# Optimization experiments

Hardware: AMD Instinct MI355X
Metric: run time of the kernel (lower is better)

## Reference

```python
import jax, jax.numpy as jnp
import numpy as np

EMBED_DIM = 1024
HEAD_DIM = 64
B, S = 16, 2048


def setup_inputs() -> dict:
    key = jax.random.key(0)
    ks = jax.random.split(key, 8)
    scale = 1.0 / np.sqrt(EMBED_DIM)
    return {
        "x": jax.random.normal(ks[0], (B, S, EMBED_DIM), dtype=jnp.float32),
        "mask": jax.random.randint(ks[1], (B, S), 0, 2, dtype=jnp.int32),
        "Wq": jax.random.normal(ks[2], (EMBED_DIM, HEAD_DIM), dtype=jnp.float32) * scale,
        "bq": jnp.zeros((HEAD_DIM,), dtype=jnp.float32),
        "Wk": jax.random.normal(ks[3], (EMBED_DIM, HEAD_DIM), dtype=jnp.float32) * scale,
        "bk": jnp.zeros((HEAD_DIM,), dtype=jnp.float32),
        "Wv": jax.random.normal(ks[4], (EMBED_DIM, HEAD_DIM), dtype=jnp.float32) * scale,
        "bv": jnp.zeros((HEAD_DIM,), dtype=jnp.float32),
    }


def reference(x, mask, Wq, bq, Wk, bk, Wv, bv):
    # x: [B,S,E], mask: [B,S] with 0 = masked, 1 = keep
    q = x @ Wq + bq          # [B,S,D]
    k = x @ Wk + bk          # [B,S,D]
    v = x @ Wv + bv          # [B,S,D]
    scores = jnp.einsum("bsd,btd->bst", q, k) / jnp.sqrt(jnp.float32(HEAD_DIM))
    scores = jnp.where(mask[:, None, :] == 0, jnp.float32(-1e9), scores)
    attn = jax.nn.softmax(scores, axis=-1)  # [B,S,S]
    return jnp.einsum("bst,btd->bsd", attn, v)  # [B,S,D]
```

## Files before the change

### kernel.cpp

```cpp
#include <hip/hip_runtime.h>
#include <math.h>

#define EMBED 1024
#define HDIM  64
#define BATCH 16
#define SEQ   2048
#define MTOT  (BATCH*SEQ)
#define NE    (MTOT*HDIM)

typedef _Float16 f16;
typedef __attribute__((ext_vector_type(8))) _Float16 half8;
typedef __attribute__((ext_vector_type(4))) _Float16 half4;
typedef __attribute__((ext_vector_type(4))) float  float4v;

__global__ void wprep_kernel(const float* __restrict__ Wq, const float* __restrict__ Wk,
                             const float* __restrict__ Wv, f16* __restrict__ Wt)
{
    int e = blockIdx.x * 256 + threadIdx.x;
    if (e >= 192 * EMBED) return;
    int gn = e >> 10, k = e & 1023;
    int mat = gn >> 6, n = gn & 63;
    const float* W = (mat == 0) ? Wq : ((mat == 1) ? Wk : Wv);
    Wt[e] = (f16)W[k * HDIM + n];
}

__global__ __launch_bounds__(256)
void qkv_mfma_kernel(const float* __restrict__ X, const f16* __restrict__ Wt,
                     const float* __restrict__ bq, const float* __restrict__ bk, const float* __restrict__ bv,
                     f16* __restrict__ Q, f16* __restrict__ K, f16* __restrict__ Vt)
{
    __shared__ f16 Xs[64 * 72];
    __shared__ f16 Csv[64 * 72];

    const int tid  = threadIdx.x;
    const int wave = tid >> 6;
    const int lane = tid & 63;
    const int quad = lane >> 4;
    const int c16  = lane & 15;
    const int m0   = blockIdx.x * 64;
    const int gnb  = wave * 3;

    float4v acc[4][3];
    #pragma unroll
    for (int mt = 0; mt < 4; ++mt)
        #pragma unroll
        for (int nt = 0; nt < 3; ++nt)
            acc[mt][nt] = (float4v){0.f, 0.f, 0.f, 0.f};

    float4 pf[4];
    #pragma unroll
    for (int i = 0; i < 4; ++i) {
        int c = tid + 256 * i, m = c >> 4, ko = (c & 15) * 4;
        pf[i] = *(const float4*)(X + (size_t)(m0 + m) * EMBED + ko);
    }

    for (int k0 = 0; k0 < EMBED; k0 += 64) {
        half8 bh[2][3];
        #pragma unroll
        for (int ks = 0; ks < 2; ++ks)
            #pragma unroll
            for (int nt = 0; nt < 3; ++nt)
                bh[ks][nt] = *(const half8*)(Wt + (size_t)((gnb + nt) * 16 + c16) * EMBED
                                             + k0 + ks * 32 + quad * 8);

        __syncthreads();
        #pragma unroll
        for (int i = 0; i < 4; ++i) {
            int c = tid + 256 * i, m = c >> 4, ko = (c & 15) * 4;
            half4 h = { (f16)pf[i].x, (f16)pf[i].y, (f16)pf[i].z, (f16)pf[i].w };
            *(half4*)&Xs[m * 72 + ko] = h;
        }
        __syncthreads();

        {
            int k1 = (k0 + 64) & (EMBED - 1);
            #pragma unroll
            for (int i = 0; i < 4; ++i) {
                int c = tid + 256 * i, m = c >> 4, ko = (c & 15) * 4;
                pf[i] = *(const float4*)(X + (size_t)(m0 + m) * EMBED + k1 + ko);
            }
        }

        #pragma unroll
        for (int ks = 0; ks < 2; ++ks) {
            half8 a[4];
            #pragma unroll
            for (int mt = 0; mt < 4; ++mt)
                a[mt] = *(const half8*)&Xs[(mt * 16 + c16) * 72 + ks * 32 + quad * 8];
            #pragma unroll
            for (int mt = 0; mt < 4; ++mt)
                #pragma unroll
                for (int nt = 0; nt < 3; ++nt)
                    acc[mt][nt] = __builtin_amdgcn_mfma_f32_16x16x32_f16(a[mt], bh[ks][nt], acc[mt][nt], 0, 0, 0);
        }
    }

    float bb[3];
    #pragma unroll
    for (int nt = 0; nt < 3; ++nt) {
        int gn = (gnb + nt) * 16 + c16, mat = gn >> 6, cn = gn & 63;
        bb[nt] = ((mat == 0) ? bq : ((mat == 1) ? bk : bv))[cn];
    }

    #pragma unroll
    for (int mt = 0; mt < 4; ++mt)
        #pragma unroll
        for (int nt = 0; nt < 3; ++nt) {
            int gn = (gnb + nt) * 16 + c16, mat = gn >> 6, cn = gn & 63;
            if (mat < 2) {
                f16* O = mat ? K : Q;
                #pragma unroll
                for (int r = 0; r < 4; ++r)
                    O[(size_t)(m0 + mt * 16 + quad * 4 + r) * HDIM + cn] =
                        (f16)(acc[mt][nt][r] + bb[nt]);
            }
        }

    __syncthreads();
    #pragma unroll
    for (int mt = 0; mt < 4; ++mt)
        #pragma unroll
        for (int nt = 0; nt < 3; ++nt) {
            int gn = (gnb + nt) * 16 + c16, mat = gn >> 6, cn = gn & 63;
            if (mat == 2) {
                #pragma unroll
                for (int r = 0; r < 4; ++r)
                    Csv[cn * 72 + mt * 16 + quad * 4 + r] = (f16)(acc[mt][nt][r] + bb[nt]);
            }
        }
    __syncthreads();
    {
        int d = tid >> 2, ms = (tid & 3) * 16;
        #pragma unroll
        for (int j = 0; j < 2; ++j)
            *(half8*)(Vt + (size_t)d * MTOT + m0 + ms + 8 * j) =
                *(const half8*)&Csv[d * 72 + ms + 8 * j];
    }
}

__global__ __launch_bounds__(256)
void attn_mfma_kernel(const f16* __restrict__ Q, const f16* __restrict__ K,
                      const f16* __restrict__ Vt, const int* __restrict__ mask,
                      float* __restrict__ out)
{
    __shared__ f16 Ks[64 * 72];
    __shared__ f16 Vs[64 * 72];
    __shared__ f16 Ps[4 * 16 * 72];
    __shared__ int maskS[64];

    const int tid  = threadIdx.x;
    const int wave = tid >> 6;
    const int lane = tid & 63;
    const int quad = lane >> 4;
    const int c16  = lane & 15;
    const int b    = blockIdx.y;
    const int s0   = blockIdx.x * 64;
    const int q0   = s0 + wave * 16;

    const size_t qrow = (size_t)(b * SEQ + q0 + c16) * HDIM;
    half8 qa0 = *(const half8*)(Q + qrow + quad * 8);
    half8 qa1 = *(const half8*)(Q + qrow + 32 + quad * 8);

    const half8 ones = { (f16)1.f, (f16)1.f, (f16)1.f, (f16)1.f,
                         (f16)1.f, (f16)1.f, (f16)1.f, (f16)1.f };

    float4v O[4];
    #pragma unroll
    for (int dt = 0; dt < 4; ++dt) O[dt] = (float4v){0.f, 0.f, 0.f, 0.f};
    float4v lacc = (float4v){0.f, 0.f, 0.f, 0.f};

    const size_t kbase = (size_t)b * SEQ * HDIM;
    const int vcol0 = b * SEQ;
    const int pbase = wave * 16 * 72;

    half8 pfK[2], pfV[2];
    int mreg;
    #pragma unroll
    for (int i = 0; i < 2; ++i) {
        int c = tid + 256 * i, j = c >> 3, o = (c & 7) * 8;
        pfK[i] = *(const half8*)(K  + kbase + (size_t)j * HDIM + o);
        pfV[i] = *(const half8*)(Vt + (size_t)j * MTOT + vcol0 + o);
    }
    mreg = mask[b * SEQ + (tid & 63)];

    for (int t0 = 0; t0 < SEQ; t0 += 64) {
        __syncthreads();
        #pragma unroll
        for (int i = 0; i < 2; ++i) {
            int c = tid + 256 * i, j = c >> 3, o = (c & 7) * 8;
            *(half8*)&Ks[j * 72 + o] = pfK[i];
            *(half8*)&Vs[j * 72 + o] = pfV[i];
        }
        if (tid < 64) maskS[tid] = mreg;
        __syncthreads();

        {
            int t1 = (t0 + 64) & (SEQ - 1);
            #pragma unroll
            for (int i = 0; i < 2; ++i) {
                int c = tid + 256 * i, j = c >> 3, o = (c & 7) * 8;
                pfK[i] = *(const half8*)(K  + kbase + (size_t)(t1 + j) * HDIM + o);
                pfV[i] = *(const half8*)(Vt + (size_t)j * MTOT + vcol0 + t1 + o);
            }
            mreg = mask[b * SEQ + t1 + (tid & 63)];
        }

        float4v s[4];
        #pragma unroll
        for (int nt = 0; nt < 4; ++nt) {
            const int krow = (nt * 16 + c16) * 72;
            half8 kh0 = *(const half8*)&Ks[krow + quad * 8];
            half8 kh1 = *(const half8*)&Ks[krow + 32 + quad * 8];
            float4v a = (float4v){0.f, 0.f, 0.f, 0.f};
            a = __builtin_amdgcn_mfma_f32_16x16x32_f16(qa0, kh0, a, 0, 0, 0);
            a = __builtin_amdgcn_mfma_f32_16x16x32_f16(qa1, kh1, a, 0, 0, 0);
            s[nt] = a;
        }

        #pragma unroll
        for (int nt = 0; nt < 4; ++nt) {
            int mk = maskS[nt * 16 + c16];
            #pragma unroll
            for (int r = 0; r < 4; ++r) {
                float t = fmaf(s[nt][r], 0.125f, -6.0f);
                t = mk ? t : -1e30f;
                Ps[pbase + (quad * 4 + r) * 72 + nt * 16 + c16] = (f16)__expf(t);
            }
        }

        const int prow = pbase + c16 * 72;
        half8 pa0 = *(const half8*)&Ps[prow + quad * 8];
        half8 pa1 = *(const half8*)&Ps[prow + 32 + quad * 8];
        lacc = __builtin_amdgcn_mfma_f32_16x16x32_f16(pa0, ones, lacc, 0, 0, 0);
        lacc = __builtin_amdgcn_mfma_f32_16x16x32_f16(pa1, ones, lacc, 0, 0, 0);
        #pragma unroll
        for (int dt = 0; dt < 4; ++dt) {
            const int vrow = (dt * 16 + c16) * 72;
            half8 vh0 = *(const half8*)&Vs[vrow + quad * 8];
            half8 vh1 = *(const half8*)&Vs[vrow + 32 + quad * 8];
            O[dt] = __builtin_amdgcn_mfma_f32_16x16x32_f16(pa0, vh0, O[dt], 0, 0, 0);
            O[dt] = __builtin_amdgcn_mfma_f32_16x16x32_f16(pa1, vh1, O[dt], 0, 0, 0);
        }
    }

    #pragma unroll
    for (int r = 0; r < 4; ++r) {
        float inv = 1.0f / lacc[r];
        size_t orow = (size_t)(b * SEQ + q0 + quad * 4 + r) * HDIM;
        #pragma unroll
        for (int dt = 0; dt < 4; ++dt)
            out[orow + dt * 16 + c16] = O[dt][r] * inv;
    }
}

extern "C" void kernel_launch(void* const* d_in, const int* in_sizes, int n_in,
                              void* d_out, int out_size, void* d_ws, size_t ws_size,
                              hipStream_t stream) {
    const float* x    = (const float*)d_in[0];
    const int*   mask = (const int*)  d_in[1];
    const float* Wq   = (const float*)d_in[2];
    const float* bq   = (const float*)d_in[3];
    const float* Wk   = (const float*)d_in[4];
    const float* bk   = (const float*)d_in[5];
    const float* Wv   = (const float*)d_in[6];
    const float* bv   = (const float*)d_in[7];
    float* out = (float*)d_out;

    f16* Qf = (f16*)d_ws;
    f16* Kf = Qf + (size_t)NE;
    f16* Vt = Kf + (size_t)NE;
    f16* Wt = Vt + (size_t)NE;

    wprep_kernel<<<dim3(768), dim3(256), 0, stream>>>(Wq, Wk, Wv, Wt);

    qkv_mfma_kernel<<<dim3(MTOT / 64), dim3(256), 0, stream>>>(
        x, Wt, bq, bk, bv, Qf, Kf, Vt);

    attn_mfma_kernel<<<dim3(SEQ / 64, BATCH), dim3(256), 0, stream>>>(
        Qf, Kf, Vt, mask, out);
}
```

Before: 261.4 us.

## Give each attention wave two query tiles and double-buffer K/V in LDS

The attention kernel drops from 4 waves of 16 query rows to 2 waves of 32 rows each, so every K/V fragment read from LDS feeds two MFMA tiles. K/V shared buffers are double-buffered, which removes one of the two block barriers per key tile. The mask now lives in registers and is broadcast with wave shuffles instead of going through LDS. The cost is higher register pressure per wave, fewer waves per block (so less latency hiding), and more LDS use.

```diff
diff --git a/kernel.cpp b/kernel.cpp
--- a/kernel.cpp
+++ b/kernel.cpp
@@ -138,15 +138,14 @@
     }
 }
 
-__global__ __launch_bounds__(256)
+__global__ __launch_bounds__(128)
 void attn_mfma_kernel(const f16* __restrict__ Q, const f16* __restrict__ K,
                       const f16* __restrict__ Vt, const int* __restrict__ mask,
                       float* __restrict__ out)
 {
-    __shared__ f16 Ks[64 * 72];
-    __shared__ f16 Vs[64 * 72];
-    __shared__ f16 Ps[4 * 16 * 72];
-    __shared__ int maskS[64];
+    __shared__ f16 Ks[2][64 * 72];
+    __shared__ f16 Vs[2][64 * 72];
+    __shared__ f16 Ps[2][32 * 72];
 
     const int tid  = threadIdx.x;
     const int wave = tid >> 6;
@@ -155,102 +154,131 @@
     const int c16  = lane & 15;
     const int b    = blockIdx.y;
     const int s0   = blockIdx.x * 64;
-    const int q0   = s0 + wave * 16;
-
-    const size_t qrow = (size_t)(b * SEQ + q0 + c16) * HDIM;
-    half8 qa0 = *(const half8*)(Q + qrow + quad * 8);
-    half8 qa1 = *(const half8*)(Q + qrow + 32 + quad * 8);
+    const int q0   = s0 + wave * 32;
+
+    half8 qa[2][2];
+    #pragma unroll
+    for (int qt = 0; qt < 2; ++qt) {
+        const size_t qrow = (size_t)(b * SEQ + q0 + qt * 16 + c16) * HDIM;
+        qa[qt][0] = *(const half8*)(Q + qrow + quad * 8);
+        qa[qt][1] = *(const half8*)(Q + qrow + 32 + quad * 8);
+    }
 
     const half8 ones = { (f16)1.f, (f16)1.f, (f16)1.f, (f16)1.f,
                          (f16)1.f, (f16)1.f, (f16)1.f, (f16)1.f };
 
-    float4v O[4];
-    #pragma unroll
-    for (int dt = 0; dt < 4; ++dt) O[dt] = (float4v){0.f, 0.f, 0.f, 0.f};
-    float4v lacc = (float4v){0.f, 0.f, 0.f, 0.f};
+    float4v O[2][4];
+    #pragma unroll
+    for (int qt = 0; qt < 2; ++qt)
+        #pragma unroll
+        for (int dt = 0; dt < 4; ++dt) O[qt][dt] = (float4v){0.f, 0.f, 0.f, 0.f};
+    float4v lacc[2];
+    lacc[0] = (float4v){0.f, 0.f, 0.f, 0.f};
+    lacc[1] = (float4v){0.f, 0.f, 0.f, 0.f};
 
     const size_t kbase = (size_t)b * SEQ * HDIM;
     const int vcol0 = b * SEQ;
-    const int pbase = wave * 16 * 72;
-
-    half8 pfK[2], pfV[2];
-    int mreg;
-    #pragma unroll
-    for (int i = 0; i < 2; ++i) {
-        int c = tid + 256 * i, j = c >> 3, o = (c & 7) * 8;
+
+    half8 pfK[4], pfV[4];
+    #pragma unroll
+    for (int i = 0; i < 4; ++i) {
+        int c = tid + 128 * i, j = c >> 3, o = (c & 7) * 8;
         pfK[i] = *(const half8*)(K  + kbase + (size_t)j * HDIM + o);
         pfV[i] = *(const half8*)(Vt + (size_t)j * MTOT + vcol0 + o);
     }
-    mreg = mask[b * SEQ + (tid & 63)];
-
+    int mnext = mask[b * SEQ + lane];
+
+    int cur = 0;
     for (int t0 = 0; t0 < SEQ; t0 += 64) {
-        __syncthreads();
-        #pragma unroll
-        for (int i = 0; i < 2; ++i) {
-            int c = tid + 256 * i, j = c >> 3, o = (c & 7) * 8;
-            *(half8*)&Ks[j * 72 + o] = pfK[i];
-            *(half8*)&Vs[j * 72 + o] = pfV[i];
-        }
-        if (tid < 64) maskS[tid] = mreg;
-        __syncthreads();
+        #pragma unroll
+        for (int i = 0; i < 4; ++i) {
+            int c = tid + 128 * i, j = c >> 3, o = (c & 7) * 8;
+            *(half8*)&Ks[cur][j * 72 + o] = pfK[i];
+            *(half8*)&Vs[cur][j * 72 + o] = pfV[i];
+        }
+        int mcur = mnext;
 
         {
             int t1 = (t0 + 64) & (SEQ - 1);
             #pragma unroll
-            for (int i = 0; i < 2; ++i) {
-                int c = tid + 256 * i, j = c >> 3, o = (c & 7) * 8;
+            for (int i = 0; i < 4; ++i) {
+                int c = tid + 128 * i, j = c >> 3, o = (c & 7) * 8;
                 pfK[i] = *(const half8*)(K  + kbase + (size_t)(t1 + j) * HDIM + o);
                 pfV[i] = *(const half8*)(Vt + (size_t)j * MTOT + vcol0 + t1 + o);
             }
-            mreg = mask[b * SEQ + t1 + (tid & 63)];
-        }
-
-        float4v s[4];
+            mnext = mask[b * SEQ + t1 + lane];
+        }
+
+        __syncthreads();
+
+        int mk[4];
+        #pragma unroll
+        for (int nt = 0; nt < 4; ++nt) mk[nt] = __shfl(mcur, nt * 16 + c16, 64);
+
+        float4v s[2][4];
         #pragma unroll
         for (int nt = 0; nt < 4; ++nt) {
             const int krow = (nt * 16 + c16) * 72;
-            half8 kh0 = *(const half8*)&Ks[krow + quad * 8];
-            half8 kh1 = *(const half8*)&Ks[krow + 32 + quad * 8];
-            float4v a = (float4v){0.f, 0.f, 0.f, 0.f};
-            a = __builtin_amdgcn_mfma_f32_16x16x32_f16(qa0, kh0, a, 0, 0, 0);
-            a = __builtin_amdgcn_mfma_f32_16x16x32_f16(qa1, kh1, a, 0, 0, 0);
-            s[nt] = a;
-        }
-
-        #pragma unroll
-        for (int nt = 0; nt < 4; ++nt) {
-            int mk = maskS[nt * 16 + c16];
-            #pragma unroll
-            for (int r = 0; r < 4; ++r) {
-                float t = fmaf(s[nt][r], 0.125f, -6.0f);
-                t = mk ? t : -1e30f;
-                Ps[pbase + (quad * 4 + r) * 72 + nt * 16 + c16] = (f16)__expf(t);
-            }
-        }
-
-        const int prow = pbase + c16 * 72;
-        half8 pa0 = *(const half8*)&Ps[prow + quad * 8];
-        half8 pa1 = *(const half8*)&Ps[prow + 32 + quad * 8];
-        lacc = __builtin_amdgcn_mfma_f32_16x16x32_f16(pa0, ones, lacc, 0, 0, 0);
-        lacc = __builtin_amdgcn_mfma_f32_16x16x32_f16(pa1, ones, lacc, 0, 0, 0);
+            half8 kh0 = *(const half8*)&Ks[cur][krow + quad * 8];
+            half8 kh1 = *(const half8*)&Ks[cur][krow + 32 + quad * 8];
+            #pragma unroll
+            for (int qt = 0; qt < 2; ++qt) {
+                float4v a = (float4v){0.f, 0.f, 0.f, 0.f};
+                a = __builtin_amdgcn_mfma_f32_16x16x32_f16(qa[qt][0], kh0, a, 0, 0, 0);
+                a = __builtin_amdgcn_mfma_f32_16x16x32_f16(qa[qt][1], kh1, a, 0, 0, 0);
+                s[qt][nt] = a;
+            }
+        }
+
+        #pragma unroll
+        for (int qt = 0; qt < 2; ++qt)
+            #pragma unroll
+            for (int nt = 0; nt < 4; ++nt) {
+                #pragma unroll
+                for (int r = 0; r < 4; ++r) {
+                    float t = fmaf(s[qt][nt][r], 0.125f, -6.0f);
+                    t = mk[nt] ? t : -1e30f;
+                    Ps[wave][(qt * 16 + quad * 4 + r) * 72 + nt * 16 + c16] = (f16)__expf(t);
+                }
+            }
+
+        half8 pa[2][2];
+        #pragma unroll
+        for (int qt = 0; qt < 2; ++qt) {
+            const int prow = (qt * 16 + c16) * 72;
+            pa[qt][0] = *(const half8*)&Ps[wave][prow + quad * 8];
+            pa[qt][1] = *(const half8*)&Ps[wave][prow + 32 + quad * 8];
+        }
+        #pragma unroll
+        for (int qt = 0; qt < 2; ++qt) {
+            lacc[qt] = __builtin_amdgcn_mfma_f32_16x16x32_f16(pa[qt][0], ones, lacc[qt], 0, 0, 0);
+            lacc[qt] = __builtin_amdgcn_mfma_f32_16x16x32_f16(pa[qt][1], ones, lacc[qt], 0, 0, 0);
+        }
         #pragma unroll
         for (int dt = 0; dt < 4; ++dt) {
             const int vrow = (dt * 16 + c16) * 72;
-            half8 vh0 = *(const half8*)&Vs[vrow + quad * 8];
-            half8 vh1 = *(const half8*)&Vs[vrow + 32 + quad * 8];
-            O[dt] = __builtin_amdgcn_mfma_f32_16x16x32_f16(pa0, vh0, O[dt], 0, 0, 0);
-            O[dt] = __builtin_amdgcn_mfma_f32_16x16x32_f16(pa1, vh1, O[dt], 0, 0, 0);
-        }
-    }
-
-    #pragma unroll
-    for (int r = 0; r < 4; ++r) {
-        float inv = 1.0f / lacc[r];
-        size_t orow = (size_t)(b * SEQ + q0 + quad * 4 + r) * HDIM;
-        #pragma unroll
-        for (int dt = 0; dt < 4; ++dt)
-            out[orow + dt * 16 + c16] = O[dt][r] * inv;
-    }
+            half8 vh0 = *(const half8*)&Vs[cur][vrow + quad * 8];
+            half8 vh1 = *(const half8*)&Vs[cur][vrow + 32 + quad * 8];
+            #pragma unroll
+            for (int qt = 0; qt < 2; ++qt) {
+                O[qt][dt] = __builtin_amdgcn_mfma_f32_16x16x32_f16(pa[qt][0], vh0, O[qt][dt], 0, 0, 0);
+                O[qt][dt] = __builtin_amdgcn_mfma_f32_16x16x32_f16(pa[qt][1], vh1, O[qt][dt], 0, 0, 0);
+            }
+        }
+
+        cur ^= 1;
+    }
+
+    #pragma unroll
+    for (int qt = 0; qt < 2; ++qt)
+        #pragma unroll
+        for (int r = 0; r < 4; ++r) {
+            float inv = 1.0f / lacc[qt][r];
+            size_t orow = (size_t)(b * SEQ + q0 + qt * 16 + quad * 4 + r) * HDIM;
+            #pragma unroll
+            for (int dt = 0; dt < 4; ++dt)
+                out[orow + dt * 16 + c16] = O[qt][dt][r] * inv;
+        }
 }
 
 extern "C" void kernel_launch(void* const* d_in, const int* in_sizes, int n_in,
@@ -276,6 +304,6 @@
     qkv_mfma_kernel<<<dim3(MTOT / 64), dim3(256), 0, stream>>>(
         x, Wt, bq, bk, bv, Qf, Kf, Vt);
 
-    attn_mfma_kernel<<<dim3(SEQ / 64, BATCH), dim3(256), 0, stream>>>(
+    attn_mfma_kernel<<<dim3(SEQ / 64, BATCH), dim3(128), 0, stream>>>(
         Qf, Kf, Vt, mask, out);
 }
```

Result: slower. 278.6 us (+6.6%).
